# Performance work log

Hardware: AMD Instinct MI355X
Metric: run time of the kernel (lower is better)

The kernel has to match this reference:

```python
import jax, jax.numpy as jnp
import numpy as np

N_EMBD = 1024
N_HEAD = 16
HEAD_DIM = N_EMBD // N_HEAD


def setup_inputs() -> dict:
    key = jax.random.key(0)
    ks = jax.random.split(key, 5)
    x = jax.random.normal(ks[0], (2, 2048, N_EMBD), dtype=jnp.float32)
    # Linear params, scaled like torch default init (~U(-1/sqrt(fan_in),..)) approximated with small normal
    s = 1.0 / np.sqrt(N_EMBD)
    W_qkv = jax.random.normal(ks[1], (N_EMBD, 3 * N_EMBD), dtype=jnp.float32) * s
    b_qkv = jax.random.normal(ks[2], (3 * N_EMBD,), dtype=jnp.float32) * s
    W_proj = jax.random.normal(ks[3], (N_EMBD, N_EMBD), dtype=jnp.float32) * s
    b_proj = jax.random.normal(ks[4], (N_EMBD,), dtype=jnp.float32) * s
    return {"x": x, "W_qkv": W_qkv, "b_qkv": b_qkv, "W_proj": W_proj, "b_proj": b_proj}


def reference(x, W_qkv, b_qkv, W_proj, b_proj):
    B, T, C = x.shape
    qkv = x @ W_qkv + b_qkv                              # [B,T,3C]
    qkv = qkv.reshape(B, T, 3, N_HEAD, HEAD_DIM)
    qkv = jnp.transpose(qkv, (2, 0, 3, 1, 4))            # [3,B,H,T,D]
    q, k, v = qkv[0], qkv[1], qkv[2]
    scale = HEAD_DIM ** -0.5
    att = jnp.einsum('bhqd,bhkd->bhqk', q, k) * scale    # [B,H,T,T]
    causal = jnp.tril(jnp.ones((T, T), dtype=bool))
    att = jnp.where(causal, att, -jnp.inf)
    att = jax.nn.softmax(att, axis=-1)
    y = jnp.einsum('bhqk,bhkd->bhqd', att, v)            # [B,H,T,D]
    y = jnp.transpose(y, (0, 2, 1, 3)).reshape(B, T, C)
    return y @ W_proj + b_proj
```

## Files before the change

kernel.cpp:

```cpp
#include <hip/hip_runtime.h>
#include <hip/hip_bf16.h>
#include <stdint.h>

#define N_EMBD 1024
#define N_HEAD 16
#define HEAD_DIM 64
#define T_SEQ 2048
#define BATCH 2
#define M_TOK (BATCH * T_SEQ)

typedef short bf16x8 __attribute__((ext_vector_type(8)));
typedef float f32x4 __attribute__((ext_vector_type(4)));

__device__ __forceinline__ void gload_lds16(const void* g, void* l) {
  __builtin_amdgcn_global_load_lds(
      (const __attribute__((address_space(1))) void*)g,
      (__attribute__((address_space(3))) void*)l, 16, 0, 0);
}

__device__ __forceinline__ uint16_t f2bf(float x) {
  uint32_t u = __float_as_uint(x);
  uint32_t r = (u + 0x7FFFu + ((u >> 16) & 1u)) >> 16;
  return (uint16_t)r;
}

__global__ void convert_f32_bf16(const float* __restrict__ in,
                                 uint16_t* __restrict__ out, int n) {
  int i = (blockIdx.x * blockDim.x + threadIdx.x) * 4;
  int stride = gridDim.x * blockDim.x * 4;
  for (; i + 3 < n; i += stride) {
    float4 v = *(const float4*)(in + i);
    ushort4 o;
    o.x = f2bf(v.x); o.y = f2bf(v.y); o.z = f2bf(v.z); o.w = f2bf(v.w);
    *(ushort4*)(out + i) = o;
  }
}

__global__ void transpose_convert(const float* __restrict__ W,
                                  uint16_t* __restrict__ Wt, int R, int C_) {
  __shared__ uint16_t t[64][65];
  int c0 = blockIdx.x * 64, r0 = blockIdx.y * 64;
  int lc = threadIdx.x & 63, lr4 = threadIdx.x >> 6;
#pragma unroll
  for (int rr = 0; rr < 16; ++rr) {
    int r = rr * 4 + lr4;
    t[r][lc] = f2bf(W[(size_t)(r0 + r) * C_ + c0 + lc]);
  }
  __syncthreads();
#pragma unroll
  for (int rr = 0; rr < 16; ++rr) {
    int r = rr * 4 + lr4;
    Wt[(size_t)(c0 + r) * R + r0 + lc] = t[lc][r];
  }
}

__global__ void transpose_v(const uint16_t* __restrict__ qkv,
                            uint16_t* __restrict__ Vt) {
  __shared__ uint16_t t[64][65];
  int t0 = blockIdx.x * 64;
  int bh = blockIdx.y;
  int b = bh >> 4, h = bh & 15;
  int lc = threadIdx.x & 63, lr4 = threadIdx.x >> 6;
  const uint16_t* src =
      qkv + (size_t)(b * T_SEQ) * (3 * N_EMBD) + 2 * N_EMBD + h * 64;
#pragma unroll
  for (int rr = 0; rr < 16; ++rr) {
    int r = rr * 4 + lr4;
    t[r][lc] = src[(size_t)(t0 + r) * (3 * N_EMBD) + lc];
  }
  __syncthreads();
  uint16_t* dst = Vt + (size_t)bh * 64 * T_SEQ;
#pragma unroll
  for (int rr = 0; rr < 16; ++rr) {
    int d = rr * 4 + lr4;
    dst[(size_t)d * T_SEQ + t0 + lc] = t[lc][d];
  }
}

template <int OUT_BF16>
__global__ __launch_bounds__(256) void gemm_bt(
    const uint16_t* __restrict__ A, const uint16_t* __restrict__ Bt,
    const float* __restrict__ bias, void* __restrict__ Cv, int M, int N,
    int K) {
  __shared__ __attribute__((aligned(16))) uint16_t sA[2][128 * 32];
  __shared__ __attribute__((aligned(16))) uint16_t sB[2][128 * 32];
  int tid = threadIdx.x;
  int w = tid >> 6, l = tid & 63;
  int wm = w >> 1, wn = w & 1;
  int ql = l & 15, hi = l >> 4;
  size_t m0 = (size_t)blockIdx.x * 128, n0 = (size_t)blockIdx.y * 128;
  f32x4 acc[4][4] = {};

#pragma unroll
  for (int r = 0; r < 2; ++r) {
    int base = r * 256 + (w << 6);
    int idx = base + l;
    gload_lds16(A + (m0 + (idx >> 2)) * K + (idx & 3) * 8, &sA[0][0] + base * 8);
    gload_lds16(Bt + (n0 + (idx >> 2)) * K + (idx & 3) * 8, &sB[0][0] + base * 8);
  }

  int cur = 0;
  for (int kt = 0; kt < K; kt += 32) {
    if (kt + 32 < K) {
#pragma unroll
      for (int r = 0; r < 2; ++r) {
        int base = r * 256 + (w << 6);
        int idx = base + l;
        gload_lds16(A + (m0 + (idx >> 2)) * K + kt + 32 + (idx & 3) * 8,
                    &sA[cur ^ 1][0] + base * 8);
        gload_lds16(Bt + (n0 + (idx >> 2)) * K + kt + 32 + (idx & 3) * 8,
                    &sB[cur ^ 1][0] + base * 8);
      }
      asm volatile("s_waitcnt vmcnt(4)" ::: "memory");
    } else {
      asm volatile("s_waitcnt vmcnt(0)" ::: "memory");
    }
    __builtin_amdgcn_s_barrier();
    __builtin_amdgcn_sched_barrier(0);
    bf16x8 af[4], bfr[4];
#pragma unroll
    for (int i = 0; i < 4; i++)
      af[i] = *(const bf16x8*)(&sA[cur][0] + (wm * 64 + i * 16 + ql) * 32 + hi * 8);
#pragma unroll
    for (int j = 0; j < 4; j++)
      bfr[j] = *(const bf16x8*)(&sB[cur][0] + (wn * 64 + j * 16 + ql) * 32 + hi * 8);
#pragma unroll
    for (int i = 0; i < 4; i++)
#pragma unroll
      for (int j = 0; j < 4; j++)
        acc[i][j] = __builtin_amdgcn_mfma_f32_16x16x32_bf16(af[i], bfr[j],
                                                            acc[i][j], 0, 0, 0);
    __builtin_amdgcn_sched_barrier(0);
    __builtin_amdgcn_s_barrier();
    cur ^= 1;
  }

#pragma unroll
  for (int i = 0; i < 4; i++) {
    size_t m = m0 + wm * 64 + i * 16 + hi * 4;
#pragma unroll
    for (int j = 0; j < 4; j++) {
      size_t n = n0 + wn * 64 + j * 16 + ql;
      float bv = bias[n];
#pragma unroll
      for (int r = 0; r < 4; r++) {
        float v = acc[i][j][r] + bv;
        if (OUT_BF16)
          ((uint16_t*)Cv)[(m + r) * N + n] = f2bf(v);
        else
          ((float*)Cv)[(m + r) * N + n] = v;
      }
    }
  }
}

__global__ __launch_bounds__(256, 4) void attn_kernel(
    const uint16_t* __restrict__ qkv, const uint16_t* __restrict__ Vt,
    uint16_t* __restrict__ y) {
  __shared__ __attribute__((aligned(16))) uint16_t sK[2][64 * 64];
  __shared__ __attribute__((aligned(16))) uint16_t sV[2][64 * 64];

  int tid = threadIdx.x;
  int w = tid >> 6, l = tid & 63;
  int ql = l & 15, hi = l >> 4;
  int id = blockIdx.x;
  int xcd = id & 7;
  int bh = xcd * 4 + ((id >> 3) & 3);
  int qt = 31 - (id >> 5);
  int b = bh >> 4, h = bh & 15;
  const size_t rs = 3 * N_EMBD;
  const uint16_t* Qb = qkv + (size_t)(b * T_SEQ) * rs + h * 64;
  const uint16_t* Kb = Qb + N_EMBD;
  const uint16_t* Vb = Vt + (size_t)bh * 64 * T_SEQ;
  const bool lo = hi < 2;
  const int sl0 = ql + ((hi & 1) << 5);
  const int sl1 = sl0 + 16;
  const int qloc = w * 16 + ql;
  const int qg = qt * 64 + qloc;

  bf16x8 qf0 = *(const bf16x8*)(Qb + (size_t)qg * rs + hi * 8);
  bf16x8 qf1 = *(const bf16x8*)(Qb + (size_t)qg * rs + 32 + hi * 8);
#pragma unroll
  for (int j = 0; j < 8; ++j) {
    uint16_t u = (uint16_t)qf0[j];
    qf0[j] = (short)(((u & 0x7f80u) >= 0x180u) ? (u - 0x180u) : (u & 0x8000u));
    uint16_t v = (uint16_t)qf1[j];
    qf1[j] = (short)(((v & 0x7f80u) >= 0x180u) ? (v - 0x180u) : (v & 0x8000u));
  }

  f32x4 acc[4] = {};
  float m_run = -1e30f, l_part = 0.f;
  const int xr = (ql & 7) * 8;

#pragma unroll
  for (int s2 = 0; s2 < 2; ++s2) {
    int base16 = s2 * 256 + w * 64;
    int idx = base16 + l;
    int row = idx >> 3, c = idx & 7;
    int d8 = c ^ (row & 7);
    gload_lds16(Kb + (size_t)row * rs + d8 * 8, &sK[0][0] + base16 * 8);
    gload_lds16(Vb + (size_t)row * T_SEQ + 0 + d8 * 8, &sV[0][0] + base16 * 8);
  }

  int cur = 0;
  for (int t = 0; t <= qt; ++t) {
    if (t < qt) {
      const int kvn = (t + 1) << 6;
#pragma unroll
      for (int s2 = 0; s2 < 2; ++s2) {
        int base16 = s2 * 256 + w * 64;
        int idx = base16 + l;
        int row = idx >> 3, c = idx & 7;
        int d8 = c ^ (row & 7);
        gload_lds16(Kb + (size_t)(kvn + row) * rs + d8 * 8,
                    &sK[cur ^ 1][0] + base16 * 8);
        gload_lds16(Vb + (size_t)row * T_SEQ + kvn + d8 * 8,
                    &sV[cur ^ 1][0] + base16 * 8);
      }
      asm volatile("s_waitcnt vmcnt(4)" ::: "memory");
    } else {
      asm volatile("s_waitcnt vmcnt(0)" ::: "memory");
    }
    __builtin_amdgcn_s_barrier();
    __builtin_amdgcn_sched_barrier(0);
    const uint16_t* kb_l = &sK[cur][0];
    const uint16_t* vb_l = &sV[cur][0];
    f32x4 sfr[4] = {};
    __builtin_amdgcn_s_setprio(1);
#pragma unroll
    for (int f = 0; f < 4; ++f) {
      bf16x8 k0 = *(const bf16x8*)(kb_l + (16 * f + ql) * 64 + ((hi * 8) ^ xr));
      bf16x8 k1 =
          *(const bf16x8*)(kb_l + (16 * f + ql) * 64 + (((4 + hi) * 8) ^ xr));
      sfr[f] = __builtin_amdgcn_mfma_f32_16x16x32_bf16(k0, qf0, sfr[f], 0, 0, 0);
      sfr[f] = __builtin_amdgcn_mfma_f32_16x16x32_bf16(k1, qf1, sfr[f], 0, 0, 0);
    }
    __builtin_amdgcn_s_setprio(0);
    float sv[16];
    if (t == qt) {
      const int kb0 = 4 * hi;
#pragma unroll
      for (int f = 0; f < 4; ++f)
#pragma unroll
        for (int r = 0; r < 4; ++r)
          sv[4 * f + r] = (16 * f + kb0 + r <= qloc) ? sfr[f][r] : -1e30f;
    } else {
#pragma unroll
      for (int f = 0; f < 4; ++f)
#pragma unroll
        for (int r = 0; r < 4; ++r) sv[4 * f + r] = sfr[f][r];
    }
    float x0 = fmaxf(fmaxf(sv[0], sv[1]), fmaxf(sv[2], sv[3]));
    float x1 = fmaxf(fmaxf(sv[4], sv[5]), fmaxf(sv[6], sv[7]));
    float x2 = fmaxf(fmaxf(sv[8], sv[9]), fmaxf(sv[10], sv[11]));
    float x3 = fmaxf(fmaxf(sv[12], sv[13]), fmaxf(sv[14], sv[15]));
    float tmax = fmaxf(fmaxf(x0, x1), fmaxf(x2, x3));
    if (__any(tmax > m_run)) {
      float tm = fmaxf(tmax, __shfl_xor(tmax, 16));
      tm = fmaxf(tm, __shfl_xor(tm, 32));
      float m_new = fmaxf(m_run, tm);
      float corr = __expf(m_run - m_new);
      m_run = m_new;
      l_part *= corr;
#pragma unroll
      for (int d = 0; d < 4; ++d) acc[d] *= corr;
    }
    float pv[16];
#pragma unroll
    for (int i2 = 0; i2 < 16; ++i2) pv[i2] = __expf(sv[i2] - m_run);
    float s01 = (pv[0] + pv[1]) + (pv[2] + pv[3]);
    float s23 = (pv[4] + pv[5]) + (pv[6] + pv[7]);
    float s45 = (pv[8] + pv[9]) + (pv[10] + pv[11]);
    float s67 = (pv[12] + pv[13]) + (pv[14] + pv[15]);
    l_part += (s01 + s23) + (s45 + s67);
    uint32_t wp[8];
#pragma unroll
    for (int f = 0; f < 4; ++f) {
      asm("v_cvt_pk_bf16_f32 %0, %1, %2"
          : "=v"(wp[2 * f]) : "v"(pv[4 * f]), "v"(pv[4 * f + 1]));
      asm("v_cvt_pk_bf16_f32 %0, %1, %2"
          : "=v"(wp[2 * f + 1]) : "v"(pv[4 * f + 2]), "v"(pv[4 * f + 3]));
    }
    union { uint32_t u[4]; bf16x8 v; } pf0, pf1;
    {
      uint32_t a0 = __shfl((int)wp[0], sl0), b0 = __shfl((int)wp[2], sl0);
      uint32_t a1 = __shfl((int)wp[1], sl0), b1 = __shfl((int)wp[3], sl0);
      uint32_t a2 = __shfl((int)wp[0], sl1), b2 = __shfl((int)wp[2], sl1);
      uint32_t a3 = __shfl((int)wp[1], sl1), b3 = __shfl((int)wp[3], sl1);
      pf0.u[0] = lo ? a0 : b0; pf0.u[1] = lo ? a1 : b1;
      pf0.u[2] = lo ? a2 : b2; pf0.u[3] = lo ? a3 : b3;
    }
    {
      uint32_t a0 = __shfl((int)wp[4], sl0), b0 = __shfl((int)wp[6], sl0);
      uint32_t a1 = __shfl((int)wp[5], sl0), b1 = __shfl((int)wp[7], sl0);
      uint32_t a2 = __shfl((int)wp[4], sl1), b2 = __shfl((int)wp[6], sl1);
      uint32_t a3 = __shfl((int)wp[5], sl1), b3 = __shfl((int)wp[7], sl1);
      pf1.u[0] = lo ? a0 : b0; pf1.u[1] = lo ? a1 : b1;
      pf1.u[2] = lo ? a2 : b2; pf1.u[3] = lo ? a3 : b3;
    }
    __builtin_amdgcn_s_setprio(1);
#pragma unroll
    for (int d = 0; d < 4; ++d) {
      bf16x8 v0 = *(const bf16x8*)(vb_l + (16 * d + ql) * 64 + ((hi * 8) ^ xr));
      acc[d] = __builtin_amdgcn_mfma_f32_16x16x32_bf16(v0, pf0.v, acc[d], 0, 0, 0);
    }
#pragma unroll
    for (int d = 0; d < 4; ++d) {
      bf16x8 v1 =
          *(const bf16x8*)(vb_l + (16 * d + ql) * 64 + (((4 + hi) * 8) ^ xr));
      acc[d] = __builtin_amdgcn_mfma_f32_16x16x32_bf16(v1, pf1.v, acc[d], 0, 0, 0);
    }
    __builtin_amdgcn_s_setprio(0);
    __builtin_amdgcn_sched_barrier(0);
    __builtin_amdgcn_s_barrier();
    cur ^= 1;
  }

  float lt = l_part + __shfl_xor(l_part, 16);
  lt += __shfl_xor(lt, 32);
  float inv = 1.0f / lt;
  uint16_t* yrow = y + (size_t)(b * T_SEQ + qg) * N_EMBD + h * 64;
#pragma unroll
  for (int d = 0; d < 4; ++d) {
    uint32_t o01, o23;
    float v0 = acc[d][0] * inv, v1 = acc[d][1] * inv;
    float v2 = acc[d][2] * inv, v3 = acc[d][3] * inv;
    asm("v_cvt_pk_bf16_f32 %0, %1, %2" : "=v"(o01) : "v"(v0), "v"(v1));
    asm("v_cvt_pk_bf16_f32 %0, %1, %2" : "=v"(o23) : "v"(v2), "v"(v3));
    *(uint32_t*)(yrow + d * 16 + hi * 4) = o01;
    *(uint32_t*)(yrow + d * 16 + hi * 4 + 2) = o23;
  }
}

extern "C" void kernel_launch(void* const* d_in, const int* in_sizes, int n_in,
                              void* d_out, int out_size, void* d_ws,
                              size_t ws_size, hipStream_t stream) {
  const float* x = (const float*)d_in[0];
  const float* Wqkv = (const float*)d_in[1];
  const float* bqkv = (const float*)d_in[2];
  const float* Wproj = (const float*)d_in[3];
  const float* bproj = (const float*)d_in[4];
  float* out = (float*)d_out;

  uint8_t* ws = (uint8_t*)d_ws;
  uint16_t* xb = (uint16_t*)(ws);
  uint16_t* wqkvT = (uint16_t*)(ws + (8u << 20));
  uint16_t* wprojT = (uint16_t*)(ws + (14u << 20));
  uint16_t* qkv = (uint16_t*)(ws + (16u << 20));
  uint16_t* vt = (uint16_t*)(ws + (40u << 20));
  uint16_t* yb = (uint16_t*)(ws + (48u << 20));

  convert_f32_bf16<<<dim3(4096), dim3(256), 0, stream>>>(x, xb,
                                                         M_TOK * N_EMBD);
  transpose_convert<<<dim3(3072 / 64, 1024 / 64), dim3(256), 0, stream>>>(
      Wqkv, wqkvT, 1024, 3072);
  transpose_convert<<<dim3(1024 / 64, 1024 / 64), dim3(256), 0, stream>>>(
      Wproj, wprojT, 1024, 1024);
  gemm_bt<1><<<dim3(M_TOK / 128, 3072 / 128), dim3(256), 0, stream>>>(
      xb, wqkvT, bqkv, qkv, M_TOK, 3072, 1024);
  transpose_v<<<dim3(T_SEQ / 64, 32), dim3(256), 0, stream>>>(qkv, vt);
  attn_kernel<<<dim3(1024), dim3(256), 0, stream>>>(qkv, vt, yb);
  gemm_bt<0><<<dim3(M_TOK / 128, 1024 / 128), dim3(256), 0, stream>>>(
      yb, wprojT, bproj, out, M_TOK, 1024, 1024);
}
```

Measured before the change: 126.1 us.

## Process two query tiles per attention block to reuse K/V tiles

Each attention workgroup now handles two adjacent 64-row query tiles (128 queries), sharing every K/V tile loaded into LDS across both, and the grid is halved to 512 blocks. K and V fragments are read from LDS once into registers and fed to MFMAs for both query sets, with the first tile skipping the final diagonal step. The aim is to halve K/V global and LDS traffic per query. The cost is more registers, with launch bounds lowered to 2 blocks per CU, fewer blocks, and coarser causal load imbalance.

```diff
diff --git a/kernel.cpp b/kernel.cpp
--- a/kernel.cpp
+++ b/kernel.cpp
@@ -154,7 +154,110 @@
   }
 }
 
-__global__ __launch_bounds__(256, 4) void attn_kernel(
+__device__ __forceinline__ void sm_pack(const f32x4* sfr, f32x4* acc,
+                                        float& m_run, float& l_part, bool mask,
+                                        int qloc, int hi, bool lo, int sl0,
+                                        int sl1, bf16x8& pf0o, bf16x8& pf1o) {
+  float sv[16];
+  if (mask) {
+    const int kb0 = 4 * hi;
+#pragma unroll
+    for (int f = 0; f < 4; ++f)
+#pragma unroll
+      for (int r = 0; r < 4; ++r)
+        sv[4 * f + r] = (16 * f + kb0 + r <= qloc) ? sfr[f][r] : -1e30f;
+  } else {
+#pragma unroll
+    for (int f = 0; f < 4; ++f)
+#pragma unroll
+      for (int r = 0; r < 4; ++r) sv[4 * f + r] = sfr[f][r];
+  }
+  float x0 = fmaxf(fmaxf(sv[0], sv[1]), fmaxf(sv[2], sv[3]));
+  float x1 = fmaxf(fmaxf(sv[4], sv[5]), fmaxf(sv[6], sv[7]));
+  float x2 = fmaxf(fmaxf(sv[8], sv[9]), fmaxf(sv[10], sv[11]));
+  float x3 = fmaxf(fmaxf(sv[12], sv[13]), fmaxf(sv[14], sv[15]));
+  float tmax = fmaxf(fmaxf(x0, x1), fmaxf(x2, x3));
+  if (__any(tmax > m_run)) {
+    float tm = fmaxf(tmax, __shfl_xor(tmax, 16));
+    tm = fmaxf(tm, __shfl_xor(tm, 32));
+    float m_new = fmaxf(m_run, tm);
+    float corr = __expf(m_run - m_new);
+    m_run = m_new;
+    l_part *= corr;
+#pragma unroll
+    for (int d = 0; d < 4; ++d) acc[d] *= corr;
+  }
+  float pv[16];
+#pragma unroll
+  for (int i2 = 0; i2 < 16; ++i2) pv[i2] = __expf(sv[i2] - m_run);
+  float s01 = (pv[0] + pv[1]) + (pv[2] + pv[3]);
+  float s23 = (pv[4] + pv[5]) + (pv[6] + pv[7]);
+  float s45 = (pv[8] + pv[9]) + (pv[10] + pv[11]);
+  float s67 = (pv[12] + pv[13]) + (pv[14] + pv[15]);
+  l_part += (s01 + s23) + (s45 + s67);
+  uint32_t wp[8];
+#pragma unroll
+  for (int f = 0; f < 4; ++f) {
+    asm("v_cvt_pk_bf16_f32 %0, %1, %2"
+        : "=v"(wp[2 * f]) : "v"(pv[4 * f]), "v"(pv[4 * f + 1]));
+    asm("v_cvt_pk_bf16_f32 %0, %1, %2"
+        : "=v"(wp[2 * f + 1]) : "v"(pv[4 * f + 2]), "v"(pv[4 * f + 3]));
+  }
+  union { uint32_t u[4]; bf16x8 v; } pf0, pf1;
+  {
+    uint32_t a0 = __shfl((int)wp[0], sl0), b0 = __shfl((int)wp[2], sl0);
+    uint32_t a1 = __shfl((int)wp[1], sl0), b1 = __shfl((int)wp[3], sl0);
+    uint32_t a2 = __shfl((int)wp[0], sl1), b2 = __shfl((int)wp[2], sl1);
+    uint32_t a3 = __shfl((int)wp[1], sl1), b3 = __shfl((int)wp[3], sl1);
+    pf0.u[0] = lo ? a0 : b0; pf0.u[1] = lo ? a1 : b1;
+    pf0.u[2] = lo ? a2 : b2; pf0.u[3] = lo ? a3 : b3;
+  }
+  {
+    uint32_t a0 = __shfl((int)wp[4], sl0), b0 = __shfl((int)wp[6], sl0);
+    uint32_t a1 = __shfl((int)wp[5], sl0), b1 = __shfl((int)wp[7], sl0);
+    uint32_t a2 = __shfl((int)wp[4], sl1), b2 = __shfl((int)wp[6], sl1);
+    uint32_t a3 = __shfl((int)wp[5], sl1), b3 = __shfl((int)wp[7], sl1);
+    pf1.u[0] = lo ? a0 : b0; pf1.u[1] = lo ? a1 : b1;
+    pf1.u[2] = lo ? a2 : b2; pf1.u[3] = lo ? a3 : b3;
+  }
+  pf0o = pf0.v;
+  pf1o = pf1.v;
+}
+
+__device__ __forceinline__ void load_q_scaled(const uint16_t* Qb, int qg,
+                                              int hi, bf16x8& q0, bf16x8& q1) {
+  const size_t rs = 3 * N_EMBD;
+  q0 = *(const bf16x8*)(Qb + (size_t)qg * rs + hi * 8);
+  q1 = *(const bf16x8*)(Qb + (size_t)qg * rs + 32 + hi * 8);
+#pragma unroll
+  for (int j = 0; j < 8; ++j) {
+    uint16_t u = (uint16_t)q0[j];
+    q0[j] = (short)(((u & 0x7f80u) >= 0x180u) ? (u - 0x180u) : (u & 0x8000u));
+    uint16_t v = (uint16_t)q1[j];
+    q1[j] = (short)(((v & 0x7f80u) >= 0x180u) ? (v - 0x180u) : (v & 0x8000u));
+  }
+}
+
+__device__ __forceinline__ void write_o(const f32x4* acc, float l_part,
+                                        uint16_t* y, int b, int h, int qg,
+                                        int hi) {
+  float lt = l_part + __shfl_xor(l_part, 16);
+  lt += __shfl_xor(lt, 32);
+  float inv = 1.0f / lt;
+  uint16_t* yrow = y + (size_t)(b * T_SEQ + qg) * N_EMBD + h * 64;
+#pragma unroll
+  for (int d = 0; d < 4; ++d) {
+    uint32_t o01, o23;
+    float v0 = acc[d][0] * inv, v1 = acc[d][1] * inv;
+    float v2 = acc[d][2] * inv, v3 = acc[d][3] * inv;
+    asm("v_cvt_pk_bf16_f32 %0, %1, %2" : "=v"(o01) : "v"(v0), "v"(v1));
+    asm("v_cvt_pk_bf16_f32 %0, %1, %2" : "=v"(o23) : "v"(v2), "v"(v3));
+    *(uint32_t*)(yrow + d * 16 + hi * 4) = o01;
+    *(uint32_t*)(yrow + d * 16 + hi * 4 + 2) = o23;
+  }
+}
+
+__global__ __launch_bounds__(256, 2) void attn_kernel(
     const uint16_t* __restrict__ qkv, const uint16_t* __restrict__ Vt,
     uint16_t* __restrict__ y) {
   __shared__ __attribute__((aligned(16))) uint16_t sK[2][64 * 64];
@@ -166,7 +269,7 @@
   int id = blockIdx.x;
   int xcd = id & 7;
   int bh = xcd * 4 + ((id >> 3) & 3);
-  int qt = 31 - (id >> 5);
+  int qt = 15 - (id >> 5);
   int b = bh >> 4, h = bh & 15;
   const size_t rs = 3 * N_EMBD;
   const uint16_t* Qb = qkv + (size_t)(b * T_SEQ) * rs + h * 64;
@@ -176,21 +279,17 @@
   const int sl0 = ql + ((hi & 1) << 5);
   const int sl1 = sl0 + 16;
   const int qloc = w * 16 + ql;
-  const int qg = qt * 64 + qloc;
-
-  bf16x8 qf0 = *(const bf16x8*)(Qb + (size_t)qg * rs + hi * 8);
-  bf16x8 qf1 = *(const bf16x8*)(Qb + (size_t)qg * rs + 32 + hi * 8);
-#pragma unroll
-  for (int j = 0; j < 8; ++j) {
-    uint16_t u = (uint16_t)qf0[j];
-    qf0[j] = (short)(((u & 0x7f80u) >= 0x180u) ? (u - 0x180u) : (u & 0x8000u));
-    uint16_t v = (uint16_t)qf1[j];
-    qf1[j] = (short)(((v & 0x7f80u) >= 0x180u) ? (v - 0x180u) : (v & 0x8000u));
-  }
-
-  f32x4 acc[4] = {};
-  float m_run = -1e30f, l_part = 0.f;
+  const int qgA = qt * 128 + qloc;
+  const int qgB = qgA + 64;
+
+  bf16x8 qfA0, qfA1, qfB0, qfB1;
+  load_q_scaled(Qb, qgA, hi, qfA0, qfA1);
+  load_q_scaled(Qb, qgB, hi, qfB0, qfB1);
+
+  f32x4 accA[4] = {}, accB[4] = {};
+  float mA = -1e30f, lA = 0.f, mB = -1e30f, lB = 0.f;
   const int xr = (ql & 7) * 8;
+  const int nIter = 2 * qt + 2;
 
 #pragma unroll
   for (int s2 = 0; s2 < 2; ++s2) {
@@ -203,8 +302,9 @@
   }
 
   int cur = 0;
-  for (int t = 0; t <= qt; ++t) {
-    if (t < qt) {
+  for (int t = 0; t < nIter; ++t) {
+    const bool actA = (t <= 2 * qt);
+    if (t + 1 < nIter) {
       const int kvn = (t + 1) << 6;
 #pragma unroll
       for (int s2 = 0; s2 < 2; ++s2) {
@@ -225,111 +325,62 @@
     __builtin_amdgcn_sched_barrier(0);
     const uint16_t* kb_l = &sK[cur][0];
     const uint16_t* vb_l = &sV[cur][0];
-    f32x4 sfr[4] = {};
+    bf16x8 kf[8];
+#pragma unroll
+    for (int f = 0; f < 4; ++f) {
+      kf[2 * f] = *(const bf16x8*)(kb_l + (16 * f + ql) * 64 + ((hi * 8) ^ xr));
+      kf[2 * f + 1] =
+          *(const bf16x8*)(kb_l + (16 * f + ql) * 64 + (((4 + hi) * 8) ^ xr));
+    }
+    f32x4 sA[4] = {}, sB[4] = {};
     __builtin_amdgcn_s_setprio(1);
+    if (actA) {
+#pragma unroll
+      for (int f = 0; f < 4; ++f) {
+        sA[f] = __builtin_amdgcn_mfma_f32_16x16x32_bf16(kf[2 * f], qfA0, sA[f], 0, 0, 0);
+        sA[f] = __builtin_amdgcn_mfma_f32_16x16x32_bf16(kf[2 * f + 1], qfA1, sA[f], 0, 0, 0);
+      }
+    }
 #pragma unroll
     for (int f = 0; f < 4; ++f) {
-      bf16x8 k0 = *(const bf16x8*)(kb_l + (16 * f + ql) * 64 + ((hi * 8) ^ xr));
-      bf16x8 k1 =
-          *(const bf16x8*)(kb_l + (16 * f + ql) * 64 + (((4 + hi) * 8) ^ xr));
-      sfr[f] = __builtin_amdgcn_mfma_f32_16x16x32_bf16(k0, qf0, sfr[f], 0, 0, 0);
-      sfr[f] = __builtin_amdgcn_mfma_f32_16x16x32_bf16(k1, qf1, sfr[f], 0, 0, 0);
+      sB[f] = __builtin_amdgcn_mfma_f32_16x16x32_bf16(kf[2 * f], qfB0, sB[f], 0, 0, 0);
+      sB[f] = __builtin_amdgcn_mfma_f32_16x16x32_bf16(kf[2 * f + 1], qfB1, sB[f], 0, 0, 0);
     }
     __builtin_amdgcn_s_setprio(0);
-    float sv[16];
-    if (t == qt) {
-      const int kb0 = 4 * hi;
-#pragma unroll
-      for (int f = 0; f < 4; ++f)
-#pragma unroll
-        for (int r = 0; r < 4; ++r)
-          sv[4 * f + r] = (16 * f + kb0 + r <= qloc) ? sfr[f][r] : -1e30f;
-    } else {
-#pragma unroll
-      for (int f = 0; f < 4; ++f)
-#pragma unroll
-        for (int r = 0; r < 4; ++r) sv[4 * f + r] = sfr[f][r];
-    }
-    float x0 = fmaxf(fmaxf(sv[0], sv[1]), fmaxf(sv[2], sv[3]));
-    float x1 = fmaxf(fmaxf(sv[4], sv[5]), fmaxf(sv[6], sv[7]));
-    float x2 = fmaxf(fmaxf(sv[8], sv[9]), fmaxf(sv[10], sv[11]));
-    float x3 = fmaxf(fmaxf(sv[12], sv[13]), fmaxf(sv[14], sv[15]));
-    float tmax = fmaxf(fmaxf(x0, x1), fmaxf(x2, x3));
-    if (__any(tmax > m_run)) {
-      float tm = fmaxf(tmax, __shfl_xor(tmax, 16));
-      tm = fmaxf(tm, __shfl_xor(tm, 32));
-      float m_new = fmaxf(m_run, tm);
-      float corr = __expf(m_run - m_new);
-      m_run = m_new;
-      l_part *= corr;
-#pragma unroll
-      for (int d = 0; d < 4; ++d) acc[d] *= corr;
-    }
-    float pv[16];
-#pragma unroll
-    for (int i2 = 0; i2 < 16; ++i2) pv[i2] = __expf(sv[i2] - m_run);
-    float s01 = (pv[0] + pv[1]) + (pv[2] + pv[3]);
-    float s23 = (pv[4] + pv[5]) + (pv[6] + pv[7]);
-    float s45 = (pv[8] + pv[9]) + (pv[10] + pv[11]);
-    float s67 = (pv[12] + pv[13]) + (pv[14] + pv[15]);
-    l_part += (s01 + s23) + (s45 + s67);
-    uint32_t wp[8];
-#pragma unroll
-    for (int f = 0; f < 4; ++f) {
-      asm("v_cvt_pk_bf16_f32 %0, %1, %2"
-          : "=v"(wp[2 * f]) : "v"(pv[4 * f]), "v"(pv[4 * f + 1]));
-      asm("v_cvt_pk_bf16_f32 %0, %1, %2"
-          : "=v"(wp[2 * f + 1]) : "v"(pv[4 * f + 2]), "v"(pv[4 * f + 3]));
-    }
-    union { uint32_t u[4]; bf16x8 v; } pf0, pf1;
-    {
-      uint32_t a0 = __shfl((int)wp[0], sl0), b0 = __shfl((int)wp[2], sl0);
-      uint32_t a1 = __shfl((int)wp[1], sl0), b1 = __shfl((int)wp[3], sl0);
-      uint32_t a2 = __shfl((int)wp[0], sl1), b2 = __shfl((int)wp[2], sl1);
-      uint32_t a3 = __shfl((int)wp[1], sl1), b3 = __shfl((int)wp[3], sl1);
-      pf0.u[0] = lo ? a0 : b0; pf0.u[1] = lo ? a1 : b1;
-      pf0.u[2] = lo ? a2 : b2; pf0.u[3] = lo ? a3 : b3;
-    }
-    {
-      uint32_t a0 = __shfl((int)wp[4], sl0), b0 = __shfl((int)wp[6], sl0);
-      uint32_t a1 = __shfl((int)wp[5], sl0), b1 = __shfl((int)wp[7], sl0);
-      uint32_t a2 = __shfl((int)wp[4], sl1), b2 = __shfl((int)wp[6], sl1);
-      uint32_t a3 = __shfl((int)wp[5], sl1), b3 = __shfl((int)wp[7], sl1);
-      pf1.u[0] = lo ? a0 : b0; pf1.u[1] = lo ? a1 : b1;
-      pf1.u[2] = lo ? a2 : b2; pf1.u[3] = lo ? a3 : b3;
-    }
+    bf16x8 vf[8];
+#pragma unroll
+    for (int d = 0; d < 4; ++d) {
+      vf[2 * d] = *(const bf16x8*)(vb_l + (16 * d + ql) * 64 + ((hi * 8) ^ xr));
+      vf[2 * d + 1] =
+          *(const bf16x8*)(vb_l + (16 * d + ql) * 64 + (((4 + hi) * 8) ^ xr));
+    }
+    bf16x8 pA0, pA1, pB0, pB1;
+    if (actA)
+      sm_pack(sA, accA, mA, lA, t == 2 * qt, qloc, hi, lo, sl0, sl1, pA0, pA1);
+    sm_pack(sB, accB, mB, lB, t == 2 * qt + 1, qloc, hi, lo, sl0, sl1, pB0, pB1);
     __builtin_amdgcn_s_setprio(1);
-#pragma unroll
-    for (int d = 0; d < 4; ++d) {
-      bf16x8 v0 = *(const bf16x8*)(vb_l + (16 * d + ql) * 64 + ((hi * 8) ^ xr));
-      acc[d] = __builtin_amdgcn_mfma_f32_16x16x32_bf16(v0, pf0.v, acc[d], 0, 0, 0);
-    }
-#pragma unroll
-    for (int d = 0; d < 4; ++d) {
-      bf16x8 v1 =
-          *(const bf16x8*)(vb_l + (16 * d + ql) * 64 + (((4 + hi) * 8) ^ xr));
-      acc[d] = __builtin_amdgcn_mfma_f32_16x16x32_bf16(v1, pf1.v, acc[d], 0, 0, 0);
-    }
+    if (actA) {
+#pragma unroll
+      for (int d = 0; d < 4; ++d)
+        accA[d] = __builtin_amdgcn_mfma_f32_16x16x32_bf16(vf[2 * d], pA0, accA[d], 0, 0, 0);
+#pragma unroll
+      for (int d = 0; d < 4; ++d)
+        accA[d] = __builtin_amdgcn_mfma_f32_16x16x32_bf16(vf[2 * d + 1], pA1, accA[d], 0, 0, 0);
+    }
+#pragma unroll
+    for (int d = 0; d < 4; ++d)
+      accB[d] = __builtin_amdgcn_mfma_f32_16x16x32_bf16(vf[2 * d], pB0, accB[d], 0, 0, 0);
+#pragma unroll
+    for (int d = 0; d < 4; ++d)
+      accB[d] = __builtin_amdgcn_mfma_f32_16x16x32_bf16(vf[2 * d + 1], pB1, accB[d], 0, 0, 0);
     __builtin_amdgcn_s_setprio(0);
     __builtin_amdgcn_sched_barrier(0);
     __builtin_amdgcn_s_barrier();
     cur ^= 1;
   }
 
-  float lt = l_part + __shfl_xor(l_part, 16);
-  lt += __shfl_xor(lt, 32);
-  float inv = 1.0f / lt;
-  uint16_t* yrow = y + (size_t)(b * T_SEQ + qg) * N_EMBD + h * 64;
-#pragma unroll
-  for (int d = 0; d < 4; ++d) {
-    uint32_t o01, o23;
-    float v0 = acc[d][0] * inv, v1 = acc[d][1] * inv;
-    float v2 = acc[d][2] * inv, v3 = acc[d][3] * inv;
-    asm("v_cvt_pk_bf16_f32 %0, %1, %2" : "=v"(o01) : "v"(v0), "v"(v1));
-    asm("v_cvt_pk_bf16_f32 %0, %1, %2" : "=v"(o23) : "v"(v2), "v"(v3));
-    *(uint32_t*)(yrow + d * 16 + hi * 4) = o01;
-    *(uint32_t*)(yrow + d * 16 + hi * 4 + 2) = o23;
-  }
+  write_o(accA, lA, y, b, h, qgA, hi);
+  write_o(accB, lB, y, b, h, qgB, hi);
 }
 
 extern "C" void kernel_launch(void* const* d_in, const int* in_sizes, int n_in,
@@ -359,7 +410,7 @@
   gemm_bt<1><<<dim3(M_TOK / 128, 3072 / 128), dim3(256), 0, stream>>>(
       xb, wqkvT, bqkv, qkv, M_TOK, 3072, 1024);
   transpose_v<<<dim3(T_SEQ / 64, 32), dim3(256), 0, stream>>>(qkv, vt);
-  attn_kernel<<<dim3(1024), dim3(256), 0, stream>>>(qkv, vt, yb);
+  attn_kernel<<<dim3(512), dim3(256), 0, stream>>>(qkv, vt, yb);
   gemm_bt<0><<<dim3(M_TOK / 128, 1024 / 128), dim3(256), 0, stream>>>(
       yb, wprojT, bproj, out, M_TOK, 1024, 1024);
 }
```

After: 138.3 us. +9.7%, slower.
